# Kernel optimization log

Measured on AMD Instinct MI355X. Metric: run time of the kernel, lower is better.

Reference implementation:

```python
import jax, jax.numpy as jnp
import numpy as np

B, N, C = 4, 4096, 512
H = 8          # num_heads
M = 64         # num_landmarks
HD = C // H    # head_dim = 64
N_ITER = 6     # Newton-Schulz iterations (Nystromformer default)


def iterative_inv(mat):
    # mat: [B, H, M, M]; Nystromformer pseudo-inverse via Newton-Schulz.
    I = jnp.eye(mat.shape[-1], dtype=mat.dtype)
    K = mat
    # global-max initialization (original Nystromformer 'original' init)
    V = K.swapaxes(-1, -2) / (jnp.max(jnp.sum(K, axis=-2)) * jnp.max(jnp.sum(K, axis=-1)))
    for _ in range(N_ITER):
        KV = jnp.matmul(K, V)
        V = 0.25 * jnp.matmul(V, 13.0 * I - jnp.matmul(KV, 15.0 * I - jnp.matmul(KV, 7.0 * I - KV)))
    return V


def setup_inputs() -> dict:
    key = jax.random.key(0)
    k1, k2, k3, k4 = jax.random.split(key, 4)
    s = C ** -0.5
    return {
        "x": jax.random.normal(k1, (B, N, C), dtype=jnp.float32),
        "qkv_w": jax.random.normal(k2, (3 * C, C), dtype=jnp.float32) * s,
        "proj_w": jax.random.normal(k3, (C, C), dtype=jnp.float32) * s,
        "proj_b": jax.random.normal(k4, (C,), dtype=jnp.float32) * 0.01,
        "epoch": 1,
    }


def reference(x, qkv_w, proj_w, proj_b, epoch):
    b, n, c = x.shape
    hd = c // H
    qkv = (x @ qkv_w.T).reshape(b, n, 3, H, hd).transpose(2, 0, 3, 1, 4)  # [3,B,H,N,hd]
    Q, K, V = qkv[0], qkv[1], qkv[2]
    scale = 1.0 / np.sqrt(np.sqrt(hd)).astype(np.float32)
    Q = Q * scale
    K = K * scale
    # landmark pooling: mean over segments of length N // M
    Ql = Q.reshape(b, H, M, n // M, hd).mean(axis=-2)  # [B,H,M,hd]
    Kl = K.reshape(b, H, M, n // M, hd).mean(axis=-2)
    kernel_1 = jax.nn.softmax(jnp.einsum('bhnd,bhmd->bhnm', Q, Kl), axis=-1)   # [B,H,N,M]
    kernel_2 = jax.nn.softmax(jnp.einsum('bhmd,bhld->bhml', Ql, Kl), axis=-1)  # [B,H,M,M]
    kernel_3 = jax.nn.softmax(jnp.einsum('bhmd,bhnd->bhmn', Ql, K), axis=-1)   # [B,H,M,N]
    X = jnp.matmul(jnp.matmul(kernel_1, iterative_inv(kernel_2)), jnp.matmul(kernel_3, V))
    X = X.transpose(0, 2, 1, 3).reshape(b, n, c)
    return X @ proj_w.T + proj_b
```

## Files before the change

### kernel.cpp

```cpp
#include <hip/hip_runtime.h>
#include <hip/hip_bf16.h>
#include <stdint.h>

#define QSZe 8388608ull

typedef __attribute__((ext_vector_type(8))) short bf16x8;
typedef __attribute__((ext_vector_type(4))) float f32x4;
typedef const __attribute__((address_space(1))) unsigned int* gas1_t;
typedef __attribute__((address_space(3))) unsigned int* las3_t;

__device__ __forceinline__ float bf2f(unsigned short u) {
  return __uint_as_float(((unsigned int)u) << 16);
}
__device__ __forceinline__ unsigned short f2bf(float f) {
  unsigned int u = __float_as_uint(f);
  unsigned int r = (u + 0x7FFFu + ((u >> 16) & 1u)) >> 16;
  return (unsigned short)r;
}
__device__ __forceinline__ void gload_lds16(const void* g, void* l) {
  __builtin_amdgcn_global_load_lds((gas1_t)g, (las3_t)l, 16, 0, 0);
}
__device__ __forceinline__ unsigned int detect_f32(
    const unsigned short* __restrict__ raw_x) {
  int lane = threadIdx.x & 63;
  int big = 0;
#pragma unroll
  for (int i = 0; i < 4; i++) {
    int e = (raw_x[lane * 4 + i] >> 7) & 0xFF;
    big |= (e >= 0x8F) ? 1 : 0;
  }
  return (__ballot(big) != 0ull) ? 1u : 0u;
}

__global__ __launch_bounds__(256) void conv_all(
    const void* __restrict__ rx, const void* __restrict__ rwq,
    const void* __restrict__ rwp, unsigned short* __restrict__ cx,
    unsigned short* __restrict__ cwq, unsigned short* __restrict__ cwp,
    unsigned int* __restrict__ gstat) {
  int gid = blockIdx.x * 256 + threadIdx.x;
  if (gid == 0) {
    gstat[0] = 0u;
    gstat[1] = 0u;
  }
  unsigned int f = detect_f32((const unsigned short*)rx);
  const void* src;
  unsigned short* dst;
  int i8;
  if (gid < 1048576) {
    if (!f) return;
    src = rx; dst = cx; i8 = gid * 8;
  } else if (gid < 1146880) {
    src = rwq; dst = cwq; i8 = (gid - 1048576) * 8;
  } else {
    src = rwp; dst = cwp; i8 = (gid - 1146880) * 8;
  }
  if (f) {
    const float* fp = (const float*)src;
    float4 a = *(const float4*)(fp + i8);
    float4 b = *(const float4*)(fp + i8 + 4);
    unsigned short o[8] = {f2bf(a.x), f2bf(a.y), f2bf(a.z), f2bf(a.w),
                           f2bf(b.x), f2bf(b.y), f2bf(b.z), f2bf(b.w)};
    *(uint4*)(dst + i8) = *(const uint4*)o;
  } else {
    *(uint4*)(dst + i8) = *(const uint4*)((const unsigned short*)src + i8);
  }
}

__device__ __forceinline__ void mmB(const unsigned short* A_R,
                                    const unsigned short* B_T,
                                    unsigned short* out_R,
                                    unsigned short* out_T, int wave, int lane,
                                    float s, float dg, float a7,
                                    const unsigned short* Aelt) {
  const int fr = lane & 15, fq = lane >> 4;
  bf16x8 af0 = *(const bf16x8*)&A_R[(wave * 16 + fr) * 64 + fq * 8];
  bf16x8 af1 = *(const bf16x8*)&A_R[(wave * 16 + fr) * 64 + 32 + fq * 8];
  f32x4 acc[4] = {};
#pragma unroll
  for (int j = 0; j < 4; j++) {
    bf16x8 b0 = *(const bf16x8*)&B_T[(j * 16 + fr) * 64 + fq * 8];
    bf16x8 b1 = *(const bf16x8*)&B_T[(j * 16 + fr) * 64 + 32 + fq * 8];
    acc[j] = __builtin_amdgcn_mfma_f32_16x16x32_bf16(af0, b0, acc[j], 0, 0, 0);
    acc[j] = __builtin_amdgcn_mfma_f32_16x16x32_bf16(af1, b1, acc[j], 0, 0, 0);
  }
  float ael[4][4];
  if (Aelt) {
#pragma unroll
    for (int j = 0; j < 4; j++)
#pragma unroll
      for (int r = 0; r < 4; r++)
        ael[j][r] = bf2f(Aelt[(wave * 16 + fq * 4 + r) * 64 + j * 16 + fr]);
  }
#pragma unroll
  for (int j = 0; j < 4; j++) {
    int col = j * 16 + fr;
    unsigned short pack[4];
#pragma unroll
    for (int r = 0; r < 4; r++) {
      int row = wave * 16 + fq * 4 + r;
      float v = s * acc[j][r] + ((row == col) ? dg : 0.0f);
      if (Aelt) v += a7 * ael[j][r];
      unsigned short bv = f2bf(v);
      if (out_R) out_R[row * 64 + col] = bv;
      pack[r] = bv;
    }
    if (out_T)
      *(uint2*)&out_T[col * 64 + wave * 16 + fq * 4] = *(const uint2*)pack;
  }
}

__global__ __launch_bounds__(512) void qkv_gemm_mfma(
    const unsigned short* __restrict__ w, const void* __restrict__ xraw,
    const unsigned short* __restrict__ cx, unsigned short* __restrict__ qkv,
    float* __restrict__ Ql, float* __restrict__ Kl,
    unsigned short* __restrict__ Qlb, unsigned short* __restrict__ Klb) {
  __shared__ __align__(16) unsigned short At[3][128 * 64];
  __shared__ __align__(16) unsigned short Bt[3][256 * 64];
  const int t = threadIdx.x;
  const int lane = t & 63, wave = t >> 6;
  const int wf = wave >> 2, wt = wave & 3;
  const unsigned int isf = detect_f32((const unsigned short*)xraw);
  const unsigned short* xb = isf ? cx : (const unsigned short*)xraw;
  const int lin = blockIdx.x + blockIdx.y * 12;
  const int swz = (lin & 7) * 96 + (lin >> 3);
  const int f0 = (swz % 12) * 128, n0g = (swz / 12) * 256;
  const int srow = lane >> 3, skc = ((lane & 7) ^ srow) * 8;
  const int fr = lane & 15, fq = lane >> 4;
  const int rsw = fr & 7;
  f32x4 acc[4][4] = {};

  auto STAGE = [&](int p, int k0) {
#pragma unroll
    for (int s = 0; s < 2; s++) {
      int inst = wave * 2 + s;
      int row = inst * 8 + srow;
      gload_lds16(w + (size_t)(f0 + row) * 512 + k0 + skc,
                  &At[p][inst * 512]);
    }
#pragma unroll
    for (int s = 0; s < 4; s++) {
      int inst = wave * 4 + s;
      int row = inst * 8 + srow;
      gload_lds16(xb + (size_t)(n0g + row) * 512 + k0 + skc,
                  &Bt[p][inst * 512]);
    }
  };
  auto COMPUTE = [&](int p) {
#pragma unroll
    for (int kk = 0; kk < 64; kk += 32) {
      const int swo = (((kk >> 3) + fq) ^ rsw) << 3;
      bf16x8 af[4], bxf[4];
#pragma unroll
      for (int i = 0; i < 4; i++)
        af[i] = *(const bf16x8*)&At[p][(wf * 64 + i * 16 + fr) * 64 + swo];
#pragma unroll
      for (int j = 0; j < 4; j++)
        bxf[j] = *(const bf16x8*)&Bt[p][(wt * 64 + j * 16 + fr) * 64 + swo];
#pragma unroll
      for (int i = 0; i < 4; i++)
#pragma unroll
        for (int j = 0; j < 4; j++)
          acc[i][j] = __builtin_amdgcn_mfma_f32_16x16x32_bf16(
              af[i], bxf[j], acc[i][j], 0, 0, 0);
    }
  };

  STAGE(0, 0);
  STAGE(1, 64);
  int p = 0;
#pragma unroll 1
  for (int k0 = 0; k0 < 512; k0 += 64) {
    if (k0 + 128 < 512) {
      int pn = (p == 0) ? 2 : p - 1;
      STAGE(pn, k0 + 128);
      asm volatile("s_waitcnt vmcnt(12)" ::: "memory");
    } else if (k0 + 64 < 512) {
      asm volatile("s_waitcnt vmcnt(6)" ::: "memory");
    } else {
      asm volatile("s_waitcnt vmcnt(0)" ::: "memory");
    }
    asm volatile("s_barrier" ::: "memory");
    COMPUTE(p);
    asm volatile("s_barrier" ::: "memory");
    p = (p == 2) ? 0 : p + 1;
  }
  const int fbase = f0 + wf * 64;
  const int which = fbase >> 9;
  const int h = (fbase >> 6) & 7;
  const float scale = (which < 2) ? 0.3535533905932738f : 1.0f;
  const int b_ = n0g >> 12;
  const int bh = b_ * 8 + h;
  const int m_loc = ((n0g + wt * 64) & 4095) >> 6;
#pragma unroll
  for (int i = 0; i < 4; i++) {
    int d0 = i * 16 + fq * 4;
#pragma unroll
    for (int j = 0; j < 4; j++) {
      int nn = (n0g + wt * 64 + j * 16 + fr) & 4095;
      unsigned short pack[4];
#pragma unroll
      for (int r = 0; r < 4; r++) pack[r] = f2bf(acc[i][j][r] * scale);
      *(uint2*)&qkv[(size_t)which * QSZe + ((size_t)bh * 4096 + nn) * 64 +
                    d0] = *(const uint2*)pack;
    }
  }
  if (which < 2) {
    const float ps = scale * (1.0f / 64.0f);
#pragma unroll
    for (int i = 0; i < 4; i++) {
      float sm[4];
#pragma unroll
      for (int r = 0; r < 4; r++)
        sm[r] = acc[i][0][r] + acc[i][1][r] + acc[i][2][r] + acc[i][3][r];
#pragma unroll
      for (int mask = 1; mask < 16; mask <<= 1)
#pragma unroll
        for (int r = 0; r < 4; r++) sm[r] += __shfl_xor(sm[r], mask, 64);
      if (fr == 0) {
        int d0 = i * 16 + fq * 4;
        float4 v4 = make_float4(sm[0] * ps, sm[1] * ps, sm[2] * ps, sm[3] * ps);
        unsigned short pk[4] = {f2bf(v4.x), f2bf(v4.y), f2bf(v4.z), f2bf(v4.w)};
        size_t off = (size_t)bh * 4096 + m_loc * 64 + d0;
        if (which == 0) {
          *(float4*)&Ql[off] = v4;
          *(uint2*)&Qlb[off] = *(const uint2*)pk;
        } else {
          *(float4*)&Kl[off] = v4;
          *(uint2*)&Klb[off] = *(const uint2*)pk;
        }
      }
    }
  }
}

__global__ __launch_bounds__(256) void k3k2_mfma(
    const unsigned short* __restrict__ Qlb,
    const unsigned short* __restrict__ qkv, float* __restrict__ Wp,
    float* __restrict__ sp, const float* __restrict__ Ql,
    const float* __restrict__ Kl, float* __restrict__ k2,
    unsigned int* __restrict__ gstat) {
  __shared__ __align__(16) unsigned char SM[35840];
  const int t = threadIdx.x;
  const int lane = t & 63, wave = t >> 6;
  const int slab = blockIdx.x, bh = blockIdx.y;

  if (slab == 8) {
    float* KlT = (float*)SM;
    float* Ps = (float*)(SM + 16384);
#pragma unroll
    for (int i = 0; i < 16; i++) {
      int idx = i * 256 + t;
      KlT[(idx & 63) * 64 + (idx >> 6)] = Kl[bh * 4096 + idx];
    }
    __syncthreads();
    for (int r = wave * 16; r < wave * 16 + 16; r++) {
      float qv = Ql[(bh * 64 + r) * 64 + lane];
      float acc = 0.f;
#pragma unroll
      for (int k = 0; k < 64; k++)
        acc += __shfl(qv, k, 64) * KlT[k * 64 + lane];
      float mx = acc;
#pragma unroll
      for (int o = 32; o > 0; o >>= 1) mx = fmaxf(mx, __shfl_xor(mx, o, 64));
      float e = __expf(acc - mx);
      float s = e;
#pragma unroll
      for (int o = 32; o > 0; o >>= 1) s += __shfl_xor(s, o, 64);
      float p = e / s;
      k2[(bh * 64 + r) * 64 + lane] = p;
      Ps[r * 65 + lane] = p;
    }
    __syncthreads();
    float val = 0.f;
    if (t < 64) {
      for (int r = 0; r < 64; r++) val += Ps[r * 65 + t];
    } else if (t < 128) {
      int r = t - 64;
      for (int c = 0; c < 64; c++) val += Ps[r * 65 + c];
    }
    float mv = val;
#pragma unroll
    for (int o = 32; o > 0; o >>= 1) mv = fmaxf(mv, __shfl_xor(mv, o, 64));
    if (t == 0) atomicMax(gstat + 0, __float_as_uint(mv));
    if (t == 64) atomicMax(gstat + 1, __float_as_uint(mv));
    return;
  }
  unsigned short* Et = (unsigned short*)SM;
  unsigned short* Vt = (unsigned short*)(SM + 17408);
  float* scol_l = (float*)(SM + 34816);
  const int fr = lane & 15, fq = lane >> 4;
  const int n_base = slab * 512;
  const unsigned short* Kb = qkv + QSZe + (size_t)bh * 262144;
  const unsigned short* Vb = qkv + 2 * QSZe + (size_t)bh * 262144;
  const unsigned short* Qlp = Qlb + bh * 4096;

  bf16x8 qb[2][4];
#pragma unroll
  for (int h = 0; h < 2; h++)
#pragma unroll
    for (int j = 0; j < 4; j++)
      qb[h][j] = *(const bf16x8*)(Qlp + (j * 16 + fr) * 64 + h * 32 + fq * 8);

  f32x4 accW[4] = {};
  float scol[4] = {0.f, 0.f, 0.f, 0.f};

  const int vn = t & 127, vdg = t >> 7;
  uint4 vreg[4];
#pragma unroll
  for (int i = 0; i < 4; i++) {
    int d0 = (vdg + 2 * i) * 8;
    vreg[i] = *(const uint4*)(Vb + (size_t)(n_base + vn) * 64 + d0);
  }

#pragma unroll
  for (int sc = 0; sc < 4; sc++) {
    const int n0 = n_base + sc * 128;
#pragma unroll
    for (int i = 0; i < 4; i++) {
      int d0 = (vdg + 2 * i) * 8;
      const unsigned short* s = (const unsigned short*)&vreg[i];
#pragma unroll
      for (int u = 0; u < 8; u++) Vt[(d0 + u) * 136 + vn] = s[u];
    }
    uint4 vnext[4];
    if (sc < 3) {
#pragma unroll
      for (int i = 0; i < 4; i++) {
        int d0 = (vdg + 2 * i) * 8;
        vnext[i] = *(const uint4*)(Vb + (size_t)(n0 + 128 + vn) * 64 + d0);
      }
    }
    f32x4 acc[2][4] = {};
#pragma unroll
    for (int i = 0; i < 2; i++) {
      const unsigned short* Kr =
          Kb + (size_t)(n0 + wave * 32 + i * 16 + fr) * 64;
      bf16x8 a0 = *(const bf16x8*)(Kr + fq * 8);
      bf16x8 a1 = *(const bf16x8*)(Kr + 32 + fq * 8);
#pragma unroll
      for (int j = 0; j < 4; j++) {
        acc[i][j] = __builtin_amdgcn_mfma_f32_16x16x32_bf16(a0, qb[0][j],
                                                            acc[i][j], 0, 0, 0);
        acc[i][j] = __builtin_amdgcn_mfma_f32_16x16x32_bf16(a1, qb[1][j],
                                                            acc[i][j], 0, 0, 0);
      }
    }
#pragma unroll
    for (int i = 0; i < 2; i++)
#pragma unroll
      for (int j = 0; j < 4; j++) {
        unsigned short pack[4];
        float s4 = 0.f;
#pragma unroll
        for (int r = 0; r < 4; r++) {
          float e = __expf(acc[i][j][r]);
          s4 += e;
          pack[r] = f2bf(e);
        }
        scol[j] += s4;
        *(uint2*)&Et[(j * 16 + fr) * 136 + wave * 32 + i * 16 + fq * 4] =
            *(const uint2*)pack;
      }
    __syncthreads();
#pragma unroll
    for (int kk = 0; kk < 128; kk += 32) {
      bf16x8 ap = *(const bf16x8*)&Et[(wave * 16 + fr) * 136 + kk + fq * 8];
#pragma unroll
      for (int j = 0; j < 4; j++) {
        bf16x8 bv = *(const bf16x8*)&Vt[(j * 16 + fr) * 136 + kk + fq * 8];
        accW[j] =
            __builtin_amdgcn_mfma_f32_16x16x32_bf16(ap, bv, accW[j], 0, 0, 0);
      }
    }
    __syncthreads();
    if (sc < 3) {
#pragma unroll
      for (int i = 0; i < 4; i++) vreg[i] = vnext[i];
    }
  }
#pragma unroll
  for (int j = 0; j < 4; j++) {
    float s = scol[j];
    s += __shfl_xor(s, 16, 64);
    s += __shfl_xor(s, 32, 64);
    if (fq == 0) scol_l[wave * 64 + j * 16 + fr] = s;
  }
  __syncthreads();
  if (t < 64)
    sp[(bh * 8 + slab) * 64 + t] = scol_l[0 * 64 + t] + scol_l[1 * 64 + t] +
                                   scol_l[2 * 64 + t] + scol_l[3 * 64 + t];
  float* wpo = Wp + ((size_t)bh * 8 + slab) * 4096;
#pragma unroll
  for (int j = 0; j < 4; j++)
#pragma unroll
    for (int r = 0; r < 4; r++)
      wpo[(wave * 16 + fq * 4 + r) * 64 + j * 16 + fr] = accW[j][r];
}

__global__ __launch_bounds__(256) void ns_kernel(
    const float* __restrict__ k2g, const unsigned int* __restrict__ gstat,
    const float* __restrict__ Wp, const float* __restrict__ sp,
    unsigned short* __restrict__ Ztb) {
  __shared__ __align__(16) unsigned short L[8 * 4096];
  __shared__ float ssum[64];
  unsigned short* K2R = L;
  unsigned short* VR = L + 4096;
  unsigned short* VT = L + 2 * 4096;
  unsigned short* AR = L + 3 * 4096;
  unsigned short* AT = L + 4 * 4096;
  unsigned short* T2T = L + 5 * 4096;
  unsigned short* T3T = L + 6 * 4096;
  unsigned short* WT = L + 7 * 4096;
  const int t = threadIdx.x, bh = blockIdx.x;
  const int lane = t & 63, wave = t >> 6;
  const float scale =
      1.0f / (__uint_as_float(gstat[0]) * __uint_as_float(gstat[1]));
  const float* k2p = k2g + bh * 4096;
  if (t < 64) {
    float s = 0.f;
#pragma unroll
    for (int c = 0; c < 8; c++) s += sp[(bh * 8 + c) * 64 + t];
    ssum[t] = s;
  }
  __syncthreads();
#pragma unroll
  for (int i = 0; i < 16; i++) {
    int idx = i * 256 + t;
    int m = idx >> 6, d = idx & 63;
    float kv = k2p[idx];
    K2R[idx] = f2bf(kv);
    VT[idx] = f2bf(kv * scale);
    VR[idx] = f2bf(k2p[d * 64 + m] * scale);
    float wv = 0.f;
#pragma unroll
    for (int cc = 0; cc < 8; cc++)
      wv += Wp[((size_t)(bh * 8 + cc)) * 4096 + idx];
    WT[d * 64 + m] = f2bf(wv / ssum[m]);
  }
  __syncthreads();
  for (int it = 0; it < 6; it++) {
    mmB(K2R, VT, AR, AT, wave, lane, 1.0f, 0.0f, 0.0f, nullptr);
    __syncthreads();
    mmB(AR, AT, nullptr, T2T, wave, lane, 1.0f, 15.0f, -7.0f, AR);
    __syncthreads();
    mmB(AR, T2T, nullptr, T3T, wave, lane, -1.0f, 13.0f, 0.0f, nullptr);
    __syncthreads();
    mmB(VR, T3T, VR, VT, wave, lane, 0.25f, 0.0f, 0.0f, nullptr);
    __syncthreads();
  }
  {
    const int fr = lane & 15, fq = lane >> 4;
    bf16x8 af0 = *(const bf16x8*)&WT[(wave * 16 + fr) * 64 + fq * 8];
    bf16x8 af1 = *(const bf16x8*)&WT[(wave * 16 + fr) * 64 + 32 + fq * 8];
    f32x4 acc[4] = {};
#pragma unroll
    for (int j = 0; j < 4; j++) {
      bf16x8 b0 = *(const bf16x8*)&VR[(j * 16 + fr) * 64 + fq * 8];
      bf16x8 b1 = *(const bf16x8*)&VR[(j * 16 + fr) * 64 + 32 + fq * 8];
      acc[j] =
          __builtin_amdgcn_mfma_f32_16x16x32_bf16(af0, b0, acc[j], 0, 0, 0);
      acc[j] =
          __builtin_amdgcn_mfma_f32_16x16x32_bf16(af1, b1, acc[j], 0, 0, 0);
    }
#pragma unroll
    for (int j = 0; j < 4; j++) {
      int m = j * 16 + fr;
#pragma unroll
      for (int r = 0; r < 4; r++) {
        int d = wave * 16 + fq * 4 + r;
        Ztb[bh * 4096 + d * 64 + m] = f2bf(acc[j][r]);
      }
    }
  }
}

__global__ __launch_bounds__(256) void k1x_mfma(
    const unsigned short* __restrict__ qkv,
    const unsigned short* __restrict__ Klb,
    const unsigned short* __restrict__ Ztb, unsigned short* __restrict__ X) {
  __shared__ __align__(16) unsigned short Qt[128 * 64];
  __shared__ __align__(16) unsigned short Ps[128 * 72];
  const int t = threadIdx.x;
  const int lane = t & 63, wave = t >> 6;
  const int fr = lane & 15, fq = lane >> 4;
  const int rsw = fr & 7;
  const int bh = blockIdx.x;
  const int n0 = blockIdx.y * 128;
  const unsigned short* Qb = qkv + (size_t)bh * 262144 + (size_t)n0 * 64;
  const unsigned short* Klp = Klb + bh * 4096;
  const unsigned short* Ztp = Ztb + bh * 4096;

  {
    const int srow = lane >> 3, skc = ((lane & 7) ^ srow) * 8;
#pragma unroll
    for (int s = 0; s < 4; s++) {
      int inst = wave * 4 + s;
      gload_lds16(Qb + (size_t)(inst * 8 + srow) * 64 + skc, &Qt[inst * 512]);
    }
  }
  __syncthreads();

  f32x4 acc[2][4] = {};
#pragma unroll
  for (int kk = 0; kk < 64; kk += 32) {
    bf16x8 af[2], bg[4];
#pragma unroll
    for (int i = 0; i < 2; i++)
      af[i] = *(const bf16x8*)&Qt[(wave * 32 + i * 16 + fr) * 64 +
                                  ((((kk >> 3) + fq) ^ rsw) << 3)];
#pragma unroll
    for (int j = 0; j < 4; j++)
      bg[j] = *(const bf16x8*)(Klp + (j * 16 + fr) * 64 + kk + fq * 8);
#pragma unroll
    for (int i = 0; i < 2; i++)
#pragma unroll
      for (int j = 0; j < 4; j++)
        acc[i][j] = __builtin_amdgcn_mfma_f32_16x16x32_bf16(af[i], bg[j],
                                                            acc[i][j], 0, 0, 0);
  }

#pragma unroll
  for (int i = 0; i < 2; i++) {
    float sr[4] = {0.f, 0.f, 0.f, 0.f};
#pragma unroll
    for (int j = 0; j < 4; j++)
#pragma unroll
      for (int r = 0; r < 4; r++) {
        float e = __expf(acc[i][j][r]);
        acc[i][j][r] = e;
        sr[r] += e;
      }
#pragma unroll
    for (int mask = 1; mask < 16; mask <<= 1)
#pragma unroll
      for (int r = 0; r < 4; r++) sr[r] += __shfl_xor(sr[r], mask, 64);
    float is[4];
#pragma unroll
    for (int r = 0; r < 4; r++) is[r] = 1.0f / sr[r];
#pragma unroll
    for (int j = 0; j < 4; j++)
#pragma unroll
      for (int r = 0; r < 4; r++)
        Ps[(wave * 32 + i * 16 + fq * 4 + r) * 72 + j * 16 + fr] =
            f2bf(acc[i][j][r] * is[r]);
  }
  __syncthreads();

  f32x4 ax[2][4] = {};
#pragma unroll
  for (int kk = 0; kk < 64; kk += 32) {
    bf16x8 ap[2], bz[4];
#pragma unroll
    for (int i = 0; i < 2; i++)
      ap[i] =
          *(const bf16x8*)&Ps[(wave * 32 + i * 16 + fr) * 72 + kk + fq * 8];
#pragma unroll
    for (int j = 0; j < 4; j++)
      bz[j] = *(const bf16x8*)(Ztp + (j * 16 + fr) * 64 + kk + fq * 8);
#pragma unroll
    for (int i = 0; i < 2; i++)
#pragma unroll
      for (int j = 0; j < 4; j++)
        ax[i][j] = __builtin_amdgcn_mfma_f32_16x16x32_bf16(ap[i], bz[j],
                                                           ax[i][j], 0, 0, 0);
  }

  const int b_ = bh >> 3, h = bh & 7;
#pragma unroll
  for (int i = 0; i < 2; i++) {
#pragma unroll
    for (int j = 0; j < 4; j++) {
      int c = h * 64 + j * 16 + fr;
#pragma unroll
      for (int r = 0; r < 4; r++) {
        int n = n0 + wave * 32 + i * 16 + fq * 4 + r;
        X[((size_t)(b_ * 4096 + n)) * 512 + c] = f2bf(ax[i][j][r]);
      }
    }
  }
}

__global__ __launch_bounds__(256) void proj_gemm_mfma(
    const unsigned short* __restrict__ X, const unsigned short* __restrict__ w,
    const unsigned short* __restrict__ raw_x, const void* __restrict__ raw_b,
    float* __restrict__ out) {
  __shared__ __align__(16) unsigned short At[2][128 * 64];
  __shared__ __align__(16) unsigned short Bt[2][128 * 64];
  const int t = threadIdx.x;
  const unsigned int f = detect_f32(raw_x);
  const int lane = t & 63, wave = t >> 6;
  const int wr = wave >> 1, wc = wave & 1;
  const int i0 = blockIdx.y * 128, j0 = blockIdx.x * 128;
  const int srow = lane >> 3;
  const int skc = ((lane & 7) ^ srow) * 8;
  const int fr = lane & 15, fq = lane >> 4;
  const int rsw = fr & 7;
  f32x4 acc[4][4] = {};

  auto STAGE = [&](int p, int k0) {
#pragma unroll
    for (int s = 0; s < 4; s++) {
      int inst = wave * 4 + s;
      int row = inst * 8 + srow;
      gload_lds16(X + (size_t)(i0 + row) * 512 + k0 + skc,
                  &At[p][inst * 512]);
      gload_lds16(w + (size_t)(j0 + row) * 512 + k0 + skc,
                  &Bt[p][inst * 512]);
    }
  };
  auto COMPUTE = [&](int p) {
#pragma unroll
    for (int kk = 0; kk < 64; kk += 32) {
      const int swo = (((kk >> 3) + fq) ^ rsw) << 3;
      bf16x8 af[4], bg[4];
#pragma unroll
      for (int i = 0; i < 4; i++)
        af[i] = *(const bf16x8*)&At[p][(wr * 64 + i * 16 + fr) * 64 + swo];
#pragma unroll
      for (int j = 0; j < 4; j++)
        bg[j] = *(const bf16x8*)&Bt[p][(wc * 64 + j * 16 + fr) * 64 + swo];
#pragma unroll
      for (int i = 0; i < 4; i++)
#pragma unroll
        for (int j = 0; j < 4; j++)
          acc[i][j] = __builtin_amdgcn_mfma_f32_16x16x32_bf16(
              af[i], bg[j], acc[i][j], 0, 0, 0);
    }
  };

  STAGE(0, 0);
  int p = 0;
#pragma unroll 1
  for (int k0 = 0; k0 < 512; k0 += 64) {
    if (k0 + 64 < 512) {
      STAGE(p ^ 1, k0 + 64);
      asm volatile("s_waitcnt vmcnt(8)" ::: "memory");
    } else {
      asm volatile("s_waitcnt vmcnt(0)" ::: "memory");
    }
    asm volatile("s_barrier" ::: "memory");
    COMPUTE(p);
    asm volatile("s_barrier" ::: "memory");
    p ^= 1;
  }
#pragma unroll
  for (int j = 0; j < 4; j++) {
    int col = j0 + wc * 64 + j * 16 + fr;
    float bia = f ? ((const float*)raw_b)[col]
                  : bf2f(((const unsigned short*)raw_b)[col]);
#pragma unroll
    for (int i = 0; i < 4; i++) {
      int rbase = i0 + wr * 64 + i * 16 + fq * 4;
#pragma unroll
      for (int r = 0; r < 4; r++) {
        out[(size_t)(rbase + r) * 512 + col] = acc[i][j][r] + bia;
      }
    }
  }
}

extern "C" void kernel_launch(void* const* d_in, const int* in_sizes, int n_in,
                              void* d_out, int out_size, void* d_ws,
                              size_t ws_size, hipStream_t stream) {
  (void)in_sizes; (void)n_in; (void)out_size; (void)ws_size;

  char* w8 = (char*)d_ws;
  unsigned short* cx  = (unsigned short*)(w8 + 0);
  unsigned short* cwq = (unsigned short*)(w8 + 16777216);
  unsigned short* cwp = (unsigned short*)(w8 + 18350080);
  unsigned short* qkv = (unsigned short*)(w8 + 18876416);
  unsigned short* X   = (unsigned short*)(w8 + 69208064);
  float* Ql = (float*)(w8 + 85985280);
  float* Kl = (float*)(w8 + 86509568);
  float* k2 = (float*)(w8 + 87033856);
  unsigned short* Ztb = (unsigned short*)(w8 + 88082432);
  unsigned int* gstat = (unsigned int*)(w8 + 88606720);
  float* Wp = (float*)(w8 + 88608768);
  float* sp = (float*)(w8 + 92803072);
  unsigned short* Klb = (unsigned short*)(w8 + 92868608);
  unsigned short* Qlb = (unsigned short*)(w8 + 93130752);

  conv_all<<<4608, 256, 0, stream>>>(d_in[0], d_in[1], d_in[2], cx, cwq, cwp,
                                     gstat);
  qkv_gemm_mfma<<<dim3(12, 64), 512, 0, stream>>>(cwq, d_in[0], cx, qkv, Ql,
                                                  Kl, Qlb, Klb);
  k3k2_mfma<<<dim3(9, 32), 256, 0, stream>>>(Qlb, qkv, Wp, sp, Ql, Kl, k2,
                                             gstat);
  ns_kernel<<<32, 256, 0, stream>>>(k2, gstat, Wp, sp, Ztb);
  k1x_mfma<<<dim3(32, 32), 256, 0, stream>>>(qkv, Klb, Ztb, X);
  proj_gemm_mfma<<<dim3(4, 128), 256, 0, stream>>>(
      X, cwp, (const unsigned short*)d_in[0], d_in[3], (float*)d_out);
}
```

Baseline: 228.3 us.

## Use double-buffered QKV GEMM and atomically reduce k3 partials

The QKV GEMM drops from triple to double buffering, cutting LDS use from about 144KB to 96KB. This may allow more residency but shortens prefetch depth to one stage. Separately, the k3k2 kernel now accumulates its per-slab W and column-sum partials with float atomics into zeroed buffers (zeroed in conv_all). The NS kernel then reads a single reduced tile instead of summing 8 partials. The atomics add contention and make the summation order nondeterministic.

```diff
diff --git a/kernel.cpp b/kernel.cpp
--- a/kernel.cpp
+++ b/kernel.cpp
@@ -36,12 +36,15 @@
     const void* __restrict__ rx, const void* __restrict__ rwq,
     const void* __restrict__ rwp, unsigned short* __restrict__ cx,
     unsigned short* __restrict__ cwq, unsigned short* __restrict__ cwp,
-    unsigned int* __restrict__ gstat) {
+    unsigned int* __restrict__ gstat, float* __restrict__ Wz,
+    float* __restrict__ ssumg) {
   int gid = blockIdx.x * 256 + threadIdx.x;
   if (gid == 0) {
     gstat[0] = 0u;
     gstat[1] = 0u;
   }
+  if (gid < 131072) Wz[gid] = 0.f;
+  if (gid < 2048) ssumg[gid] = 0.f;
   unsigned int f = detect_f32((const unsigned short*)rx);
   const void* src;
   unsigned short* dst;
@@ -114,8 +117,8 @@
     const unsigned short* __restrict__ cx, unsigned short* __restrict__ qkv,
     float* __restrict__ Ql, float* __restrict__ Kl,
     unsigned short* __restrict__ Qlb, unsigned short* __restrict__ Klb) {
-  __shared__ __align__(16) unsigned short At[3][128 * 64];
-  __shared__ __align__(16) unsigned short Bt[3][256 * 64];
+  __shared__ __align__(16) unsigned short At[2][128 * 64];
+  __shared__ __align__(16) unsigned short Bt[2][256 * 64];
   const int t = threadIdx.x;
   const int lane = t & 63, wave = t >> 6;
   const int wf = wave >> 2, wt = wave & 3;
@@ -166,15 +169,11 @@
   };
 
   STAGE(0, 0);
-  STAGE(1, 64);
   int p = 0;
 #pragma unroll 1
   for (int k0 = 0; k0 < 512; k0 += 64) {
-    if (k0 + 128 < 512) {
-      int pn = (p == 0) ? 2 : p - 1;
-      STAGE(pn, k0 + 128);
-      asm volatile("s_waitcnt vmcnt(12)" ::: "memory");
-    } else if (k0 + 64 < 512) {
+    if (k0 + 64 < 512) {
+      STAGE(p ^ 1, k0 + 64);
       asm volatile("s_waitcnt vmcnt(6)" ::: "memory");
     } else {
       asm volatile("s_waitcnt vmcnt(0)" ::: "memory");
@@ -182,7 +181,7 @@
     asm volatile("s_barrier" ::: "memory");
     COMPUTE(p);
     asm volatile("s_barrier" ::: "memory");
-    p = (p == 2) ? 0 : p + 1;
+    p ^= 1;
   }
   const int fbase = f0 + wf * 64;
   const int which = fbase >> 9;
@@ -235,8 +234,8 @@
 
 __global__ __launch_bounds__(256) void k3k2_mfma(
     const unsigned short* __restrict__ Qlb,
-    const unsigned short* __restrict__ qkv, float* __restrict__ Wp,
-    float* __restrict__ sp, const float* __restrict__ Ql,
+    const unsigned short* __restrict__ qkv, float* __restrict__ Wz,
+    float* __restrict__ ssumg, const float* __restrict__ Ql,
     const float* __restrict__ Kl, float* __restrict__ k2,
     unsigned int* __restrict__ gstat) {
   __shared__ __align__(16) unsigned char SM[35840];
@@ -387,19 +386,20 @@
   }
   __syncthreads();
   if (t < 64)
-    sp[(bh * 8 + slab) * 64 + t] = scol_l[0 * 64 + t] + scol_l[1 * 64 + t] +
-                                   scol_l[2 * 64 + t] + scol_l[3 * 64 + t];
-  float* wpo = Wp + ((size_t)bh * 8 + slab) * 4096;
+    atomicAdd(&ssumg[bh * 64 + t], scol_l[0 * 64 + t] + scol_l[1 * 64 + t] +
+                                       scol_l[2 * 64 + t] + scol_l[3 * 64 + t]);
+  float* wpo = Wz + (size_t)bh * 4096;
 #pragma unroll
   for (int j = 0; j < 4; j++)
 #pragma unroll
     for (int r = 0; r < 4; r++)
-      wpo[(wave * 16 + fq * 4 + r) * 64 + j * 16 + fr] = accW[j][r];
+      atomicAdd(&wpo[(wave * 16 + fq * 4 + r) * 64 + j * 16 + fr],
+                accW[j][r]);
 }
 
 __global__ __launch_bounds__(256) void ns_kernel(
     const float* __restrict__ k2g, const unsigned int* __restrict__ gstat,
-    const float* __restrict__ Wp, const float* __restrict__ sp,
+    const float* __restrict__ Wz, const float* __restrict__ ssumg,
     unsigned short* __restrict__ Ztb) {
   __shared__ __align__(16) unsigned short L[8 * 4096];
   __shared__ float ssum[64];
@@ -416,12 +416,7 @@
   const float scale =
       1.0f / (__uint_as_float(gstat[0]) * __uint_as_float(gstat[1]));
   const float* k2p = k2g + bh * 4096;
-  if (t < 64) {
-    float s = 0.f;
-#pragma unroll
-    for (int c = 0; c < 8; c++) s += sp[(bh * 8 + c) * 64 + t];
-    ssum[t] = s;
-  }
+  if (t < 64) ssum[t] = ssumg[bh * 64 + t];
   __syncthreads();
 #pragma unroll
   for (int i = 0; i < 16; i++) {
@@ -431,10 +426,7 @@
     K2R[idx] = f2bf(kv);
     VT[idx] = f2bf(kv * scale);
     VR[idx] = f2bf(k2p[d * 64 + m] * scale);
-    float wv = 0.f;
-#pragma unroll
-    for (int cc = 0; cc < 8; cc++)
-      wv += Wp[((size_t)(bh * 8 + cc)) * 4096 + idx];
+    float wv = Wz[(size_t)bh * 4096 + idx];
     WT[d * 64 + m] = f2bf(wv / ssum[m]);
   }
   __syncthreads();
@@ -675,18 +667,18 @@
   float* k2 = (float*)(w8 + 87033856);
   unsigned short* Ztb = (unsigned short*)(w8 + 88082432);
   unsigned int* gstat = (unsigned int*)(w8 + 88606720);
-  float* Wp = (float*)(w8 + 88608768);
-  float* sp = (float*)(w8 + 92803072);
+  float* Wz = (float*)(w8 + 88608768);
+  float* ssumg = (float*)(w8 + 89133056);
   unsigned short* Klb = (unsigned short*)(w8 + 92868608);
   unsigned short* Qlb = (unsigned short*)(w8 + 93130752);
 
   conv_all<<<4608, 256, 0, stream>>>(d_in[0], d_in[1], d_in[2], cx, cwq, cwp,
-                                     gstat);
+                                     gstat, Wz, ssumg);
   qkv_gemm_mfma<<<dim3(12, 64), 512, 0, stream>>>(cwq, d_in[0], cx, qkv, Ql,
                                                   Kl, Qlb, Klb);
-  k3k2_mfma<<<dim3(9, 32), 256, 0, stream>>>(Qlb, qkv, Wp, sp, Ql, Kl, k2,
+  k3k2_mfma<<<dim3(9, 32), 256, 0, stream>>>(Qlb, qkv, Wz, ssumg, Ql, Kl, k2,
                                              gstat);
-  ns_kernel<<<32, 256, 0, stream>>>(k2, gstat, Wp, sp, Ztb);
+  ns_kernel<<<32, 256, 0, stream>>>(k2, gstat, Wz, ssumg, Ztb);
   k1x_mfma<<<dim3(32, 32), 256, 0, stream>>>(qkv, Klb, Ztb, X);
   proj_gemm_mfma<<<dim3(4, 128), 256, 0, stream>>>(
       X, cwp, (const unsigned short*)d_in[0], d_in[3], (float*)d_out);
```

After: 229.5 us. Within noise of the previous version (+0.5%).
